# Performance work log

Hardware: AMD Instinct MI355X
Metric: run time of the kernel (lower is better)

The kernel has to match this reference:

```python
import jax, jax.numpy as jnp
import numpy as np

# SuperposedExpert: K parallel TT-factorized FFN paths + holographic routing.
# d_model=1024 factorized as [32,32]; d_ff=4096 as [64,64]; tt_ranks=[1,16,1] (r0/r2 squeezed).
K, D_MODEL, D_FF, RANK = 4, 1024, 4096, 16
IN1, IN2 = 32, 32          # factorize_for_tt(d_model)
F1, F2 = 64, 64            # factorize_for_tt(d_ff)
TEMP = 1.0                 # routing_temperature


def setup_inputs() -> dict:
    key = jax.random.key(0)
    ks = jax.random.split(key, 8)
    s = 0.05
    tokens = jax.random.normal(ks[0], (2048, D_MODEL), dtype=jnp.float32)
    # TT cores for ffn1: d_model -> d_ff  (input_dims [32,32], output_dims [64,64])
    ffn1_core1 = jax.random.normal(ks[1], (K, IN1, F1, RANK), dtype=jnp.float32) * s
    ffn1_core2 = jax.random.normal(ks[2], (K, RANK, IN2, F2), dtype=jnp.float32) * s
    # TT cores for ffn2: d_ff -> d_model (input_dims [64,64], output_dims [32,32])
    ffn2_core1 = jax.random.normal(ks[3], (K, F1, IN1, RANK), dtype=jnp.float32) * s
    ffn2_core2 = jax.random.normal(ks[4], (K, RANK, F2, IN2), dtype=jnp.float32) * s
    # Holographic routing params (hd_dim == d_model -> identity HD projection)
    pb = jax.random.normal(ks[5], (K, D_MODEL), dtype=jnp.float32)
    path_bases = pb / jnp.linalg.norm(pb, axis=-1, keepdims=True)  # orthogonal-ish init
    path_weights = jax.random.normal(ks[6], (K, D_MODEL), dtype=jnp.float32) * s
    return {
        'tokens': tokens,
        'ffn1_core1': ffn1_core1, 'ffn1_core2': ffn1_core2,
        'ffn2_core1': ffn2_core1, 'ffn2_core2': ffn2_core2,
        'path_bases': path_bases, 'path_weights': path_weights,
    }


def reference(tokens, ffn1_core1, ffn1_core2, ffn2_core1, ffn2_core2,
              path_bases, path_weights):
    N = tokens.shape[0]
    # ---- K superposed TT-FFN paths ----
    x3 = tokens.reshape(N, IN1, IN2)  # [n, a, b]
    # TT matmul 1: y[x,y] = sum_{a,b,r} G1[a,x,r] G2[r,b,y] x[a,b]
    h = jnp.einsum('nab,kaxr,krby->knxy', x3, ffn1_core1, ffn1_core2)
    h = jax.nn.gelu(h.reshape(K, N, D_FF))  # quantum_activation stand-in
    h3 = h.reshape(K, N, F1, F2)
    y = jnp.einsum('knab,kaxr,krby->knxy', h3, ffn2_core1, ffn2_core2)
    y = y.reshape(K, N, D_MODEL)  # per-path outputs
    # ---- Holographic HD routing (hd_dim == d_model: identity projection) ----
    logits = jnp.einsum('nd,kd->nk', tokens, path_bases) / TEMP
    gates = jax.nn.softmax(logits, axis=-1)  # [n, k]
    # Collapse superposition: per-path elementwise HD modulation + gated sum
    out = jnp.einsum('knd,kd,nk->nd', y, 1.0 + path_weights, gates)
    return out
```

## Files before the change

### kernel.cpp

```cpp
#include <hip/hip_runtime.h>
#include <stdint.h>

#define GAS __attribute__((address_space(1)))
#define LAS __attribute__((address_space(3)))

typedef __attribute__((ext_vector_type(8))) short short8;
typedef __attribute__((ext_vector_type(16))) float f32x16;
typedef __attribute__((ext_vector_type(4))) float f32x4;

static constexpr int N_TOK = 2048;
static constexpr int DM    = 1024;
static constexpr int DF    = 4096;
static constexpr int KP    = 4;

__device__ inline unsigned short f2bf(float f) {
  union { float f; uint32_t u; } v; v.f = f;
  uint32_t u = v.u;
  u += 0x7FFFu + ((u >> 16) & 1u);
  return (unsigned short)(u >> 16);
}

__device__ inline uint32_t pk_bf(float lo, float hi) {
  union { float f; uint32_t u; } a, b; a.f = lo; b.f = hi;
  uint32_t ul = a.u + 0x7FFFu + ((a.u >> 16) & 1u);
  uint32_t uh = b.u + 0x7FFFu + ((b.u >> 16) & 1u);
  return (ul >> 16) | (uh & 0xFFFF0000u);
}

__device__ inline float gelu_gate(float v, float g) {
  float t0 = v * v;
  float u  = v * __builtin_fmaf(t0, -0.10294456f, -2.3022539f);
  float e  = __builtin_amdgcn_exp2f(u);
  float r  = __builtin_amdgcn_rcpf(1.0f + e);
  return v * g * r;
}

__device__ inline void gld16(const void* g, void* l) {
  __builtin_amdgcn_global_load_lds((const GAS void*)g, (LAS void*)l, 16, 0, 0);
}

__global__ __launch_bounds__(256) void setup_kernel(
    const float* __restrict__ tokens, const float* __restrict__ pb,
    const float* __restrict__ c11, const float* __restrict__ c12,
    const float* __restrict__ c21, const float* __restrict__ c22,
    float* __restrict__ gates, unsigned short* __restrict__ xb,
    unsigned short* __restrict__ w1t, unsigned short* __restrict__ w2t) {
  __shared__ __align__(16) float sh[17472];
  const int blk = blockIdx.x;
  const int t = threadIdx.x;
  if (blk < 1024) {
    const int k = blk >> 8, x = (blk >> 2) & 63, y0 = (blk & 3) * 16;
    float* s1  = sh;
    float* s2T = sh + 512;
    if (t < 128) {
      int a = t >> 2, rq = (t & 3) * 4;
      *(float4*)(s1 + a * 16 + rq) =
          *(const float4*)(c11 + (((size_t)(k * 32 + a)) * 64 + x) * 16 + rq);
    }
#pragma unroll
    for (int j = 0; j < 8; ++j) {
      int i = t + j * 256;
      int rb = i >> 2, yy0 = (i & 3) * 4;
      float4 v = *(const float4*)(c12 + (size_t)(k * 16) * 2048 + (size_t)rb * 64 + y0 + yy0);
      s2T[(yy0 + 0) * 524 + rb] = v.x;
      s2T[(yy0 + 1) * 524 + rb] = v.y;
      s2T[(yy0 + 2) * 524 + rb] = v.z;
      s2T[(yy0 + 3) * 524 + rb] = v.w;
    }
    __syncthreads();
    const int a = t >> 3, b0 = (t & 7) * 4;
    float4 s1q[4];
#pragma unroll
    for (int q = 0; q < 4; ++q) s1q[q] = *(const float4*)(s1 + a * 16 + q * 4);
    const float* a0s = (const float*)s1q;
    for (int y = 0; y < 16; ++y) {
      const float* s2y = s2T + y * 524;
      float4 acc = {0.f, 0.f, 0.f, 0.f};
#pragma unroll
      for (int r = 0; r < 16; ++r) {
        float cv = a0s[r];
        float4 bv = *(const float4*)(s2y + r * 32 + b0);
        acc.x = __builtin_fmaf(cv, bv.x, acc.x);
        acc.y = __builtin_fmaf(cv, bv.y, acc.y);
        acc.z = __builtin_fmaf(cv, bv.z, acc.z);
        acc.w = __builtin_fmaf(cv, bv.w, acc.w);
      }
      ushort4 o; o.x = f2bf(acc.x); o.y = f2bf(acc.y); o.z = f2bf(acc.z); o.w = f2bf(acc.w);
      *(ushort4*)(w1t + ((size_t)k * DF + x * 64 + y0 + y) * DM + t * 4) = o;
    }
  } else if (blk < 1280) {
    const int bb = blk - 1024;
    const int k = bb >> 6, x = (bb >> 1) & 31, y0 = (bb & 1) * 16;
    float* s1  = sh;
    float* s2T = sh + 1024;
    {
      int a = t >> 2, rq = (t & 3) * 4;
      *(float4*)(s1 + a * 16 + rq) =
          *(const float4*)(c21 + (((size_t)(k * 64 + a)) * 32 + x) * 16 + rq);
    }
#pragma unroll
    for (int j = 0; j < 16; ++j) {
      int i = t + j * 256;
      int rb = i >> 2, yy0 = (i & 3) * 4;
      float4 v = *(const float4*)(c22 + (size_t)(k * 16) * 2048 + (size_t)rb * 32 + y0 + yy0);
      s2T[(yy0 + 0) * 1028 + rb] = v.x;
      s2T[(yy0 + 1) * 1028 + rb] = v.y;
      s2T[(yy0 + 2) * 1028 + rb] = v.z;
      s2T[(yy0 + 3) * 1028 + rb] = v.w;
    }
    __syncthreads();
    const int b0 = (t & 15) * 4;
#pragma unroll
    for (int jj = 0; jj < 4; ++jj) {
      const int a = (t >> 4) + jj * 16;
      float4 s1q[4];
#pragma unroll
      for (int q = 0; q < 4; ++q) s1q[q] = *(const float4*)(s1 + a * 16 + q * 4);
      const float* a0s = (const float*)s1q;
      for (int y = 0; y < 16; ++y) {
        const float* s2y = s2T + y * 1028;
        float4 acc = {0.f, 0.f, 0.f, 0.f};
#pragma unroll
        for (int r = 0; r < 16; ++r) {
          float cv = a0s[r];
          float4 bv = *(const float4*)(s2y + r * 64 + b0);
          acc.x = __builtin_fmaf(cv, bv.x, acc.x);
          acc.y = __builtin_fmaf(cv, bv.y, acc.y);
          acc.z = __builtin_fmaf(cv, bv.z, acc.z);
          acc.w = __builtin_fmaf(cv, bv.w, acc.w);
        }
        ushort4 o; o.x = f2bf(acc.x); o.y = f2bf(acc.y); o.z = f2bf(acc.z); o.w = f2bf(acc.w);
        *(ushort4*)(w2t + ((size_t)k * DM + x * 32 + y0 + y) * DF + t * 4 + jj * 1024) = o;
      }
    }
  } else {
    const int wave = t >> 6, lane = t & 63;
    const int n = (blk - 1280) * 4 + wave;
    float s0 = 0.f, s1v = 0.f, s2v = 0.f, s3v = 0.f;
    const float4* tr = (const float4*)(tokens + (size_t)n * DM);
#pragma unroll
    for (int j = 0; j < 4; ++j) {
      int idx = j * 64 + lane;
      float4 tv = tr[idx];
      ushort4 b;
      b.x = f2bf(tv.x); b.y = f2bf(tv.y); b.z = f2bf(tv.z); b.w = f2bf(tv.w);
      *(ushort4*)(xb + (size_t)n * DM + idx * 4) = b;
      float4 q;
      q = ((const float4*)(pb + 0 * DM))[idx]; s0  += tv.x*q.x + tv.y*q.y + tv.z*q.z + tv.w*q.w;
      q = ((const float4*)(pb + 1 * DM))[idx]; s1v += tv.x*q.x + tv.y*q.y + tv.z*q.z + tv.w*q.w;
      q = ((const float4*)(pb + 2 * DM))[idx]; s2v += tv.x*q.x + tv.y*q.y + tv.z*q.z + tv.w*q.w;
      q = ((const float4*)(pb + 3 * DM))[idx]; s3v += tv.x*q.x + tv.y*q.y + tv.z*q.z + tv.w*q.w;
    }
#pragma unroll
    for (int off = 32; off > 0; off >>= 1) {
      s0  += __shfl_xor(s0, off);
      s1v += __shfl_xor(s1v, off);
      s2v += __shfl_xor(s2v, off);
      s3v += __shfl_xor(s3v, off);
    }
    if (lane == 0) {
      float m = fmaxf(fmaxf(s0, s1v), fmaxf(s2v, s3v));
      float e0 = __expf(s0 - m), e1 = __expf(s1v - m), e2 = __expf(s2v - m), e3 = __expf(s3v - m);
      float inv = 1.0f / (e0 + e1 + e2 + e3);
      float4 g; g.x = e0 * inv; g.y = e1 * inv; g.z = e2 * inv; g.w = e3 * inv;
      *(float4*)(gates + n * 4) = g;
    }
  }
}

#define PH_SYNC(V) do { \
    asm volatile("s_waitcnt vmcnt(" #V ")" ::: "memory"); \
    __builtin_amdgcn_s_barrier(); \
    __builtin_amdgcn_sched_barrier(0); \
  } while (0)

#define G1_TILE(KT, BO, WO, V0, V1, V2) do { \
    const int kn_ = ((KT) + 1) * 64; \
    const bool st_ = (KT) < 15; \
     \
    PH_SYNC(V0); \
    if (st_) { const unsigned short* s_ = Wg + (size_t)srow * DM + kn_ + lch * 8; \
      gld16(s_, smem + (WO) + t * 16); gld16(s_ + 64 * DM, smem + (WO) + 8192 + t * 16); } \
    _Pragma("unroll") for (int fi = 0; fi < 4; ++fi) \
      _Pragma("unroll") for (int s = 0; s < 2; ++s) \
        af[fi][s] = *(const short8*)(smem + (BO) + aRowB + fi * 2048 + (cxor16 ^ (s * 64) ^ (fi * 32))); \
    _Pragma("unroll") for (int ti = 0; ti < 2; ++ti) \
      _Pragma("unroll") for (int s = 0; s < 2; ++s) \
        bf0[ti][s] = *(const short8*)(smem + (BO) + xRowB + ti * 2048 + (cxor16 ^ (s * 64) ^ wnx64 ^ (ti * 32))); \
    __builtin_amdgcn_s_setprio(1); \
    _Pragma("unroll") for (int fi = 0; fi < 4; ++fi) \
      _Pragma("unroll") for (int ti = 0; ti < 2; ++ti) { \
        acc[0][0][fi][ti] = __builtin_amdgcn_mfma_f32_16x16x32_bf16(af[fi][0], bf0[ti][0], acc[0][0][fi][ti], 0, 0, 0); \
        acc[0][0][fi][ti] = __builtin_amdgcn_mfma_f32_16x16x32_bf16(af[fi][1], bf0[ti][1], acc[0][0][fi][ti], 0, 0, 0); } \
    __builtin_amdgcn_s_setprio(0); \
     \
    PH_SYNC(V1); \
    if (st_) { const unsigned short* s_ = Xg + (size_t)srow * DM + kn_ + lch * 8; \
      gld16(s_, smem + (WO) + 32768 + t * 16); gld16(s_ + 64 * DM, smem + (WO) + 32768 + 8192 + t * 16); } \
    _Pragma("unroll") for (int ti = 0; ti < 2; ++ti) \
      _Pragma("unroll") for (int s = 0; s < 2; ++s) \
        bf1[ti][s] = *(const short8*)(smem + (BO) + xRowB + 16384 + ti * 2048 + (cxor16 ^ (s * 64) ^ wnx64 ^ (ti * 32))); \
    __builtin_amdgcn_s_setprio(1); \
    _Pragma("unroll") for (int fi = 0; fi < 4; ++fi) \
      _Pragma("unroll") for (int ti = 0; ti < 2; ++ti) { \
        acc[0][1][fi][ti] = __builtin_amdgcn_mfma_f32_16x16x32_bf16(af[fi][0], bf1[ti][0], acc[0][1][fi][ti], 0, 0, 0); \
        acc[0][1][fi][ti] = __builtin_amdgcn_mfma_f32_16x16x32_bf16(af[fi][1], bf1[ti][1], acc[0][1][fi][ti], 0, 0, 0); } \
    __builtin_amdgcn_s_setprio(0); \
     \
    PH_SYNC(V2); \
    if (st_) { const unsigned short* s_ = Xg + (size_t)(128 + srow) * DM + kn_ + lch * 8; \
      gld16(s_, smem + (WO) + 32768 + 16384 + t * 16); gld16(s_ + 64 * DM, smem + (WO) + 32768 + 16384 + 8192 + t * 16); } \
    _Pragma("unroll") for (int fi = 0; fi < 4; ++fi) \
      _Pragma("unroll") for (int s = 0; s < 2; ++s) \
        af[fi][s] = *(const short8*)(smem + (BO) + aRowB + 16384 + fi * 2048 + (cxor16 ^ (s * 64) ^ (fi * 32))); \
    __builtin_amdgcn_s_setprio(1); \
    _Pragma("unroll") for (int fi = 0; fi < 4; ++fi) \
      _Pragma("unroll") for (int ti = 0; ti < 2; ++ti) { \
        acc[1][1][fi][ti] = __builtin_amdgcn_mfma_f32_16x16x32_bf16(af[fi][0], bf1[ti][0], acc[1][1][fi][ti], 0, 0, 0); \
        acc[1][1][fi][ti] = __builtin_amdgcn_mfma_f32_16x16x32_bf16(af[fi][1], bf1[ti][1], acc[1][1][fi][ti], 0, 0, 0); } \
    __builtin_amdgcn_s_setprio(0); \
     \
    if (st_) { const unsigned short* s_ = Wg + (size_t)(128 + srow) * DM + kn_ + lch * 8; \
      gld16(s_, smem + (WO) + 16384 + t * 16); gld16(s_ + 64 * DM, smem + (WO) + 16384 + 8192 + t * 16); } \
    __builtin_amdgcn_s_setprio(1); \
    _Pragma("unroll") for (int fi = 0; fi < 4; ++fi) \
      _Pragma("unroll") for (int ti = 0; ti < 2; ++ti) { \
        acc[1][0][fi][ti] = __builtin_amdgcn_mfma_f32_16x16x32_bf16(af[fi][0], bf0[ti][0], acc[1][0][fi][ti], 0, 0, 0); \
        acc[1][0][fi][ti] = __builtin_amdgcn_mfma_f32_16x16x32_bf16(af[fi][1], bf0[ti][1], acc[1][0][fi][ti], 0, 0, 0); } \
    __builtin_amdgcn_s_setprio(0); \
  } while (0)

__global__ __launch_bounds__(512, 1) void gemm1(
    const unsigned short* __restrict__ xb, const unsigned short* __restrict__ w1t,
    const float* __restrict__ gates, unsigned short* __restrict__ hg) {
  __shared__ __align__(16) char smem[131072];
  const int t = threadIdx.x, lane = t & 63, wv = t >> 6;
  const int wm = wv >> 2, wn = wv & 3;
  const int hw = blockIdx.x + (blockIdx.y << 3) + (blockIdx.z << 7);
  const int lg = (hw & 7) * 64 + (hw >> 3);
  const int m0 = (lg & 7) * 256;
  const int f0 = ((lg >> 3) & 15) * 256;
  const int kp = lg >> 7;
  const unsigned short* __restrict__ Wg = w1t + (size_t)kp * DF * DM + (size_t)f0 * DM;
  const unsigned short* __restrict__ Xg = xb + (size_t)m0 * DM;

  const int srow = t >> 3;
  const int lch  = (t & 7) ^ (srow & 7) ^ (srow >> 3);
  const int l15 = lane & 15, kg = lane >> 4;
  const int cxor16 = (kg ^ (lane & 7) ^ (l15 >> 3)) * 16;
  const int wnx64  = (wn & 1) * 64;
  const int aRowB  = (wm * 64 + l15) * 128;
  const int xRowB  = 32768 + (wn * 32 + l15) * 128;

  f32x4 acc[2][2][4][2] = {};
  short8 af[4][2], bf0[2][2], bf1[2][2];

  {
    const unsigned short* sw = Wg + (size_t)srow * DM + lch * 8;
    const unsigned short* sx = Xg + (size_t)srow * DM + lch * 8;
    gld16(sw,            smem + t * 16);
    gld16(sw + 64 * DM,  smem + 8192 + t * 16);
    gld16(sx,            smem + 32768 + t * 16);
    gld16(sx + 64 * DM,  smem + 32768 + 8192 + t * 16);
    gld16(sx + 128 * DM, smem + 32768 + 16384 + t * 16);
    gld16(sx + 192 * DM, smem + 32768 + 16384 + 8192 + t * 16);
    gld16(sw + 128 * DM, smem + 16384 + t * 16);
    gld16(sw + 192 * DM, smem + 16384 + 8192 + t * 16);
  }

#pragma unroll 1
  for (int kt = 0; kt < 14; kt += 2) {
    G1_TILE(kt,     0,     65536, 4, 4, 4);
    G1_TILE(kt + 1, 65536, 0,     4, 4, 4);
  }
  G1_TILE(14, 0,     65536, 4, 4, 4);
  G1_TILE(15, 65536, 0,     4, 2, 0);

  unsigned short* __restrict__ H = hg + (size_t)kp * N_TOK * DF;
#pragma unroll
  for (int cB = 0; cB < 2; ++cB)
#pragma unroll
    for (int ti = 0; ti < 2; ++ti) {
      const int tok = m0 + cB * 128 + wn * 32 + ti * 16 + l15;
      const float g = gates[tok * 4 + kp];
      unsigned short* hrow = H + (size_t)tok * DF + f0 + wm * 64 + kg * 4;
#pragma unroll
      for (int rA = 0; rA < 2; ++rA)
#pragma unroll
        for (int fi = 0; fi < 4; ++fi) {
          f32x4 v = acc[rA][cB][fi][ti];
          float r0 = gelu_gate(v.x, g);
          float r1 = gelu_gate(v.y, g);
          float r2 = gelu_gate(v.z, g);
          float r3 = gelu_gate(v.w, g);
          uint2 p; p.x = pk_bf(r0, r1); p.y = pk_bf(r2, r3);
          *(uint2*)(hrow + rA * 128 + fi * 16) = p;
        }
    }
}

#define G2_TILE(KT, BO, WO, V0, V1, V2) do { \
    const int kn_ = ((KT) + 1) * 64; \
    const bool st_ = (KT) < 63; \
     \
    PH_SYNC(V0); \
    if (st_) gld16(Wg + (size_t)srow * DF + kn_ + lch * 8, smem + (WO) + t * 16); \
    _Pragma("unroll") for (int fi = 0; fi < 2; ++fi) \
      _Pragma("unroll") for (int s = 0; s < 2; ++s) \
        af[fi][s] = *(const short8*)(smem + (BO) + awRowB + fi * 2048 + (cxor16 ^ awx ^ (fi * 32) ^ (s * 64))); \
    _Pragma("unroll") for (int ti = 0; ti < 2; ++ti) \
      _Pragma("unroll") for (int s = 0; s < 2; ++s) \
        bf0[ti][s] = *(const short8*)(smem + (BO) + xRowB + ti * 2048 + (cxor16 ^ wnx64 ^ (ti * 32) ^ (s * 64))); \
    __builtin_amdgcn_s_setprio(1); \
    _Pragma("unroll") for (int fi = 0; fi < 2; ++fi) \
      _Pragma("unroll") for (int ti = 0; ti < 2; ++ti) { \
        acc[0][0][fi][ti] = __builtin_amdgcn_mfma_f32_16x16x32_bf16(af[fi][0], bf0[ti][0], acc[0][0][fi][ti], 0, 0, 0); \
        acc[0][0][fi][ti] = __builtin_amdgcn_mfma_f32_16x16x32_bf16(af[fi][1], bf0[ti][1], acc[0][0][fi][ti], 0, 0, 0); } \
    __builtin_amdgcn_s_setprio(0); \
     \
    PH_SYNC(V1); \
    if (st_) { const unsigned short* s_ = Xg + (size_t)srow * DF + kn_ + lch * 8; \
      gld16(s_, smem + (WO) + 16384 + t * 16); gld16(s_ + 64 * DF, smem + (WO) + 16384 + 8192 + t * 16); } \
    _Pragma("unroll") for (int ti = 0; ti < 2; ++ti) \
      _Pragma("unroll") for (int s = 0; s < 2; ++s) \
        bf1[ti][s] = *(const short8*)(smem + (BO) + xRowB + 16384 + ti * 2048 + (cxor16 ^ wnx64 ^ (ti * 32) ^ (s * 64))); \
    __builtin_amdgcn_s_setprio(1); \
    _Pragma("unroll") for (int fi = 0; fi < 2; ++fi) \
      _Pragma("unroll") for (int ti = 0; ti < 2; ++ti) { \
        acc[0][1][fi][ti] = __builtin_amdgcn_mfma_f32_16x16x32_bf16(af[fi][0], bf1[ti][0], acc[0][1][fi][ti], 0, 0, 0); \
        acc[0][1][fi][ti] = __builtin_amdgcn_mfma_f32_16x16x32_bf16(af[fi][1], bf1[ti][1], acc[0][1][fi][ti], 0, 0, 0); } \
    __builtin_amdgcn_s_setprio(0); \
     \
    PH_SYNC(V2); \
    if (st_) { const unsigned short* s_ = Xg + (size_t)(128 + srow) * DF + kn_ + lch * 8; \
      gld16(s_, smem + (WO) + 32768 + t * 16); gld16(s_ + 64 * DF, smem + (WO) + 32768 + 8192 + t * 16); } \
    _Pragma("unroll") for (int fi = 0; fi < 2; ++fi) \
      _Pragma("unroll") for (int s = 0; s < 2; ++s) \
        af[fi][s] = *(const short8*)(smem + (BO) + awRowB + 8192 + fi * 2048 + (cxor16 ^ awx ^ (fi * 32) ^ (s * 64))); \
    __builtin_amdgcn_s_setprio(1); \
    _Pragma("unroll") for (int fi = 0; fi < 2; ++fi) \
      _Pragma("unroll") for (int ti = 0; ti < 2; ++ti) { \
        acc[1][1][fi][ti] = __builtin_amdgcn_mfma_f32_16x16x32_bf16(af[fi][0], bf1[ti][0], acc[1][1][fi][ti], 0, 0, 0); \
        acc[1][1][fi][ti] = __builtin_amdgcn_mfma_f32_16x16x32_bf16(af[fi][1], bf1[ti][1], acc[1][1][fi][ti], 0, 0, 0); } \
    __builtin_amdgcn_s_setprio(0); \
     \
    if (st_) gld16(Wg + (size_t)(64 + srow) * DF + kn_ + lch * 8, smem + (WO) + 8192 + t * 16); \
    __builtin_amdgcn_s_setprio(1); \
    _Pragma("unroll") for (int fi = 0; fi < 2; ++fi) \
      _Pragma("unroll") for (int ti = 0; ti < 2; ++ti) { \
        acc[1][0][fi][ti] = __builtin_amdgcn_mfma_f32_16x16x32_bf16(af[fi][0], bf0[ti][0], acc[1][0][fi][ti], 0, 0, 0); \
        acc[1][0][fi][ti] = __builtin_amdgcn_mfma_f32_16x16x32_bf16(af[fi][1], bf0[ti][1], acc[1][0][fi][ti], 0, 0, 0); } \
    __builtin_amdgcn_s_setprio(0); \
  } while (0)

__global__ __launch_bounds__(512, 1) void gemm2(
    const unsigned short* __restrict__ hg, const unsigned short* __restrict__ w2t,
    const float* __restrict__ pw, float* __restrict__ part) {
  __shared__ __align__(16) char smem[98304];
  const int t = threadIdx.x, lane = t & 63, wv = t >> 6;
  const int wm = wv >> 2, wn = wv & 3;
  const int hw = blockIdx.x + (blockIdx.y << 3) + (blockIdx.z << 6);
  const int lg = (hw & 7) * 32 + (hw >> 3);
  const int m0 = (lg & 7) * 256;
  const int n0 = ((lg >> 3) & 7) * 128;
  const int kp = lg >> 6;
  const unsigned short* __restrict__ Wg = w2t + (size_t)kp * DM * DF + (size_t)n0 * DF;
  const unsigned short* __restrict__ Xg = hg + (size_t)kp * N_TOK * DF + (size_t)m0 * DF;

  const int srow = t >> 3;
  const int lch  = (t & 7) ^ (srow & 7) ^ (srow >> 3);
  const int l15 = lane & 15, kg = lane >> 4;
  const int cxor16 = (kg ^ (lane & 7) ^ (l15 >> 3)) * 16;
  const int wnx64  = (wn & 1) * 64;
  const int awx    = wm * 64;
  const int awRowB = (wm * 32 + l15) * 128;
  const int xRowB  = 16384 + (wn * 32 + l15) * 128;

  f32x4 acc[2][2][2][2] = {};
  short8 af[2][2], bf0[2][2], bf1[2][2];

  {
    const unsigned short* sw = Wg + (size_t)srow * DF + lch * 8;
    const unsigned short* sx = Xg + (size_t)srow * DF + lch * 8;
    gld16(sw,            smem + t * 16);
    gld16(sx,            smem + 16384 + t * 16);
    gld16(sx + 64 * DF,  smem + 16384 + 8192 + t * 16);
    gld16(sx + 128 * DF, smem + 32768 + t * 16);
    gld16(sx + 192 * DF, smem + 32768 + 8192 + t * 16);
    gld16(sw + 64 * DF,  smem + 8192 + t * 16);
  }

#pragma unroll 1
  for (int kt = 0; kt < 62; kt += 2) {
    G2_TILE(kt,     0,     49152, 3, 2, 3);
    G2_TILE(kt + 1, 49152, 0,     3, 2, 3);
  }
  G2_TILE(62, 0,     49152, 3, 2, 3);
  G2_TILE(63, 49152, 0,     3, 1, 0);

  float* __restrict__ P = part + (size_t)kp * N_TOK * DM;
  float4 pwv[2][2];
#pragma unroll
  for (int rA = 0; rA < 2; ++rA)
#pragma unroll
    for (int fi = 0; fi < 2; ++fi) {
      float4 w = *(const float4*)(pw + kp * DM + n0 + rA * 64 + wm * 32 + fi * 16 + kg * 4);
      pwv[rA][fi].x = 1.0f + w.x; pwv[rA][fi].y = 1.0f + w.y;
      pwv[rA][fi].z = 1.0f + w.z; pwv[rA][fi].w = 1.0f + w.w;
    }
#pragma unroll
  for (int cB = 0; cB < 2; ++cB)
#pragma unroll
    for (int ti = 0; ti < 2; ++ti) {
      const int tok = m0 + cB * 128 + wn * 32 + ti * 16 + l15;
      float* prow = P + (size_t)tok * DM + n0 + wm * 32 + kg * 4;
#pragma unroll
      for (int rA = 0; rA < 2; ++rA)
#pragma unroll
        for (int fi = 0; fi < 2; ++fi) {
          f32x4 v = acc[rA][cB][fi][ti];
          float4 o;
          o.x = pwv[rA][fi].x * v.x;
          o.y = pwv[rA][fi].y * v.y;
          o.z = pwv[rA][fi].z * v.z;
          o.w = pwv[rA][fi].w * v.w;
          *(float4*)(prow + rA * 64 + fi * 16) = o;
        }
    }
}

__global__ __launch_bounds__(256) void reduce_k(
    const float* __restrict__ part, float* __restrict__ out) {
  const size_t i = ((size_t)blockIdx.x * 256 + threadIdx.x) * 4;
  const size_t S = (size_t)N_TOK * DM;
  float4 a = *(const float4*)(part + i);
  float4 b = *(const float4*)(part + S + i);
  float4 c = *(const float4*)(part + 2 * S + i);
  float4 d = *(const float4*)(part + 3 * S + i);
  float4 r;
  r.x = a.x + b.x + c.x + d.x;
  r.y = a.y + b.y + c.y + d.y;
  r.z = a.z + b.z + c.z + d.z;
  r.w = a.w + b.w + c.w + d.w;
  *(float4*)(out + i) = r;
}

extern "C" void kernel_launch(void* const* d_in, const int* in_sizes, int n_in,
                              void* d_out, int out_size, void* d_ws, size_t ws_size,
                              hipStream_t stream) {
  const float* tokens = (const float*)d_in[0];
  const float* f1c1   = (const float*)d_in[1];
  const float* f1c2   = (const float*)d_in[2];
  const float* f2c1   = (const float*)d_in[3];
  const float* f2c2   = (const float*)d_in[4];
  const float* pb     = (const float*)d_in[5];
  const float* pw     = (const float*)d_in[6];
  float* out = (float*)d_out;

  char* ws = (char*)d_ws;
  unsigned short* xb  = (unsigned short*)(ws);
  unsigned short* w1t = (unsigned short*)(ws + (4ull  << 20));
  float*          part = (float*)(ws + (4ull << 20));
  unsigned short* w2t = (unsigned short*)(ws + (36ull << 20));
  unsigned short* hg  = (unsigned short*)(ws + (68ull << 20));
  float*          gates = (float*)(ws + (132ull << 20));

  hipLaunchKernelGGL(setup_kernel, dim3(1792), dim3(256), 0, stream,
                     tokens, pb, f1c1, f1c2, f2c1, f2c2, gates, xb, w1t, w2t);
  hipLaunchKernelGGL(gemm1, dim3(8, 16, KP), dim3(512), 0, stream, xb, w1t, gates, hg);
  hipLaunchKernelGGL(gemm2, dim3(8, 8, KP), dim3(512), 0, stream, hg, w2t, pw, part);
  hipLaunchKernelGGL(reduce_k, dim3(2048), dim3(256), 0, stream, part, out);
}
```

Before: 243.9 us.

## Software-pipeline LDS fragment loads across phases in both GEMM kernels

Restructures the per-tile phase schedule in gemm1 and gemm2 so that the LDS fragment reads for the next phase (and the next tile's A/B fragments) are issued after the current MFMA block, not before it. The vmcnt waits and barrier placement are rearranged to match: one barrier moves to just before the third MFMA group, and a prologue preloads the first fragments. The goal is to hide LDS read latency behind MFMA execution. In exchange, register pressure goes up and the correctness of the wait counts becomes more delicate.

```diff
diff --git a/kernel.cpp b/kernel.cpp
--- a/kernel.cpp
+++ b/kernel.cpp
@@ -168,67 +168,67 @@
   }
 }
 
-#define PH_SYNC(V) do { \
-    asm volatile("s_waitcnt vmcnt(" #V ")" ::: "memory"); \
-    __builtin_amdgcn_s_barrier(); \
-    __builtin_amdgcn_sched_barrier(0); \
-  } while (0)
-
-#define G1_TILE(KT, BO, WO, V0, V1, V2) do { \
-    const int kn_ = ((KT) + 1) * 64; \
-    const bool st_ = (KT) < 15; \
-     \
-    PH_SYNC(V0); \
-    if (st_) { const unsigned short* s_ = Wg + (size_t)srow * DM + kn_ + lch * 8; \
-      gld16(s_, smem + (WO) + t * 16); gld16(s_ + 64 * DM, smem + (WO) + 8192 + t * 16); } \
+#define VMC(N) asm volatile("s_waitcnt vmcnt(" #N ")" ::: "memory")
+#define BARS do { __builtin_amdgcn_s_barrier(); __builtin_amdgcn_sched_barrier(0); } while (0)
+
+#define G1T(KT, BO, WO, V0X, V1X, DO2, PREF) do { \
+  const int kn_ = ((KT) + 1) * 64; \
+  const bool st_ = (KT) < 15; \
+   \
+  VMC(V0X); BARS; \
+  if (st_) { const unsigned short* s_ = Wg + (size_t)srow * DM + kn_ + lch * 8; \
+    gld16(s_, smem + (WO) + t * 16); gld16(s_ + 64 * DM, smem + (WO) + 8192 + t * 16); } \
+  __builtin_amdgcn_s_setprio(1); \
+  _Pragma("unroll") for (int fi = 0; fi < 4; ++fi) \
+    _Pragma("unroll") for (int ti = 0; ti < 2; ++ti) { \
+      acc[0][0][fi][ti] = __builtin_amdgcn_mfma_f32_16x16x32_bf16(af[fi][0], bf0[ti][0], acc[0][0][fi][ti], 0, 0, 0); \
+      acc[0][0][fi][ti] = __builtin_amdgcn_mfma_f32_16x16x32_bf16(af[fi][1], bf0[ti][1], acc[0][0][fi][ti], 0, 0, 0); } \
+  __builtin_amdgcn_s_setprio(0); \
+  _Pragma("unroll") for (int ti = 0; ti < 2; ++ti) \
+    _Pragma("unroll") for (int s = 0; s < 2; ++s) \
+      bf1[ti][s] = *(const short8*)(smem + (BO) + xRowB + 16384 + ti * 2048 + (cxor16 ^ (s * 64) ^ wnx64 ^ (ti * 32))); \
+   \
+  VMC(V1X); BARS; \
+  if (st_) { const unsigned short* s_ = Xg + (size_t)srow * DM + kn_ + lch * 8; \
+    gld16(s_, smem + (WO) + 32768 + t * 16); gld16(s_ + 64 * DM, smem + (WO) + 32768 + 8192 + t * 16); } \
+  __builtin_amdgcn_s_setprio(1); \
+  _Pragma("unroll") for (int fi = 0; fi < 4; ++fi) \
+    _Pragma("unroll") for (int ti = 0; ti < 2; ++ti) { \
+      acc[0][1][fi][ti] = __builtin_amdgcn_mfma_f32_16x16x32_bf16(af[fi][0], bf1[ti][0], acc[0][1][fi][ti], 0, 0, 0); \
+      acc[0][1][fi][ti] = __builtin_amdgcn_mfma_f32_16x16x32_bf16(af[fi][1], bf1[ti][1], acc[0][1][fi][ti], 0, 0, 0); } \
+  __builtin_amdgcn_s_setprio(0); \
+  _Pragma("unroll") for (int fi = 0; fi < 4; ++fi) \
+    _Pragma("unroll") for (int s = 0; s < 2; ++s) \
+      af[fi][s] = *(const short8*)(smem + (BO) + aRowB + 16384 + fi * 2048 + (cxor16 ^ (s * 64) ^ (fi * 32))); \
+   \
+  if (st_) { const unsigned short* s_ = Xg + (size_t)(128 + srow) * DM + kn_ + lch * 8; \
+    gld16(s_, smem + (WO) + 32768 + 16384 + t * 16); gld16(s_ + 64 * DM, smem + (WO) + 32768 + 16384 + 8192 + t * 16); } \
+  if (DO2) { VMC(2); } \
+  BARS; \
+  __builtin_amdgcn_s_setprio(1); \
+  _Pragma("unroll") for (int fi = 0; fi < 4; ++fi) \
+    _Pragma("unroll") for (int ti = 0; ti < 2; ++ti) { \
+      acc[1][1][fi][ti] = __builtin_amdgcn_mfma_f32_16x16x32_bf16(af[fi][0], bf1[ti][0], acc[1][1][fi][ti], 0, 0, 0); \
+      acc[1][1][fi][ti] = __builtin_amdgcn_mfma_f32_16x16x32_bf16(af[fi][1], bf1[ti][1], acc[1][1][fi][ti], 0, 0, 0); } \
+  __builtin_amdgcn_s_setprio(0); \
+   \
+  if (st_) { const unsigned short* s_ = Wg + (size_t)(128 + srow) * DM + kn_ + lch * 8; \
+    gld16(s_, smem + (WO) + 16384 + t * 16); gld16(s_ + 64 * DM, smem + (WO) + 16384 + 8192 + t * 16); } \
+  __builtin_amdgcn_s_setprio(1); \
+  _Pragma("unroll") for (int fi = 0; fi < 4; ++fi) \
+    _Pragma("unroll") for (int ti = 0; ti < 2; ++ti) { \
+      acc[1][0][fi][ti] = __builtin_amdgcn_mfma_f32_16x16x32_bf16(af[fi][0], bf0[ti][0], acc[1][0][fi][ti], 0, 0, 0); \
+      acc[1][0][fi][ti] = __builtin_amdgcn_mfma_f32_16x16x32_bf16(af[fi][1], bf0[ti][1], acc[1][0][fi][ti], 0, 0, 0); } \
+  __builtin_amdgcn_s_setprio(0); \
+  if (PREF) { \
     _Pragma("unroll") for (int fi = 0; fi < 4; ++fi) \
       _Pragma("unroll") for (int s = 0; s < 2; ++s) \
-        af[fi][s] = *(const short8*)(smem + (BO) + aRowB + fi * 2048 + (cxor16 ^ (s * 64) ^ (fi * 32))); \
+        af[fi][s] = *(const short8*)(smem + (WO) + aRowB + fi * 2048 + (cxor16 ^ (s * 64) ^ (fi * 32))); \
     _Pragma("unroll") for (int ti = 0; ti < 2; ++ti) \
       _Pragma("unroll") for (int s = 0; s < 2; ++s) \
-        bf0[ti][s] = *(const short8*)(smem + (BO) + xRowB + ti * 2048 + (cxor16 ^ (s * 64) ^ wnx64 ^ (ti * 32))); \
-    __builtin_amdgcn_s_setprio(1); \
-    _Pragma("unroll") for (int fi = 0; fi < 4; ++fi) \
-      _Pragma("unroll") for (int ti = 0; ti < 2; ++ti) { \
-        acc[0][0][fi][ti] = __builtin_amdgcn_mfma_f32_16x16x32_bf16(af[fi][0], bf0[ti][0], acc[0][0][fi][ti], 0, 0, 0); \
-        acc[0][0][fi][ti] = __builtin_amdgcn_mfma_f32_16x16x32_bf16(af[fi][1], bf0[ti][1], acc[0][0][fi][ti], 0, 0, 0); } \
-    __builtin_amdgcn_s_setprio(0); \
-     \
-    PH_SYNC(V1); \
-    if (st_) { const unsigned short* s_ = Xg + (size_t)srow * DM + kn_ + lch * 8; \
-      gld16(s_, smem + (WO) + 32768 + t * 16); gld16(s_ + 64 * DM, smem + (WO) + 32768 + 8192 + t * 16); } \
-    _Pragma("unroll") for (int ti = 0; ti < 2; ++ti) \
-      _Pragma("unroll") for (int s = 0; s < 2; ++s) \
-        bf1[ti][s] = *(const short8*)(smem + (BO) + xRowB + 16384 + ti * 2048 + (cxor16 ^ (s * 64) ^ wnx64 ^ (ti * 32))); \
-    __builtin_amdgcn_s_setprio(1); \
-    _Pragma("unroll") for (int fi = 0; fi < 4; ++fi) \
-      _Pragma("unroll") for (int ti = 0; ti < 2; ++ti) { \
-        acc[0][1][fi][ti] = __builtin_amdgcn_mfma_f32_16x16x32_bf16(af[fi][0], bf1[ti][0], acc[0][1][fi][ti], 0, 0, 0); \
-        acc[0][1][fi][ti] = __builtin_amdgcn_mfma_f32_16x16x32_bf16(af[fi][1], bf1[ti][1], acc[0][1][fi][ti], 0, 0, 0); } \
-    __builtin_amdgcn_s_setprio(0); \
-     \
-    PH_SYNC(V2); \
-    if (st_) { const unsigned short* s_ = Xg + (size_t)(128 + srow) * DM + kn_ + lch * 8; \
-      gld16(s_, smem + (WO) + 32768 + 16384 + t * 16); gld16(s_ + 64 * DM, smem + (WO) + 32768 + 16384 + 8192 + t * 16); } \
-    _Pragma("unroll") for (int fi = 0; fi < 4; ++fi) \
-      _Pragma("unroll") for (int s = 0; s < 2; ++s) \
-        af[fi][s] = *(const short8*)(smem + (BO) + aRowB + 16384 + fi * 2048 + (cxor16 ^ (s * 64) ^ (fi * 32))); \
-    __builtin_amdgcn_s_setprio(1); \
-    _Pragma("unroll") for (int fi = 0; fi < 4; ++fi) \
-      _Pragma("unroll") for (int ti = 0; ti < 2; ++ti) { \
-        acc[1][1][fi][ti] = __builtin_amdgcn_mfma_f32_16x16x32_bf16(af[fi][0], bf1[ti][0], acc[1][1][fi][ti], 0, 0, 0); \
-        acc[1][1][fi][ti] = __builtin_amdgcn_mfma_f32_16x16x32_bf16(af[fi][1], bf1[ti][1], acc[1][1][fi][ti], 0, 0, 0); } \
-    __builtin_amdgcn_s_setprio(0); \
-     \
-    if (st_) { const unsigned short* s_ = Wg + (size_t)(128 + srow) * DM + kn_ + lch * 8; \
-      gld16(s_, smem + (WO) + 16384 + t * 16); gld16(s_ + 64 * DM, smem + (WO) + 16384 + 8192 + t * 16); } \
-    __builtin_amdgcn_s_setprio(1); \
-    _Pragma("unroll") for (int fi = 0; fi < 4; ++fi) \
-      _Pragma("unroll") for (int ti = 0; ti < 2; ++ti) { \
-        acc[1][0][fi][ti] = __builtin_amdgcn_mfma_f32_16x16x32_bf16(af[fi][0], bf0[ti][0], acc[1][0][fi][ti], 0, 0, 0); \
-        acc[1][0][fi][ti] = __builtin_amdgcn_mfma_f32_16x16x32_bf16(af[fi][1], bf0[ti][1], acc[1][0][fi][ti], 0, 0, 0); } \
-    __builtin_amdgcn_s_setprio(0); \
-  } while (0)
+        bf0[ti][s] = *(const short8*)(smem + (WO) + xRowB + ti * 2048 + (cxor16 ^ (s * 64) ^ wnx64 ^ (ti * 32))); \
+  } \
+} while (0)
 
 __global__ __launch_bounds__(512, 1) void gemm1(
     const unsigned short* __restrict__ xb, const unsigned short* __restrict__ w1t,
@@ -267,14 +267,25 @@
     gld16(sw + 128 * DM, smem + 16384 + t * 16);
     gld16(sw + 192 * DM, smem + 16384 + 8192 + t * 16);
   }
+  VMC(4); BARS;
+#pragma unroll
+  for (int fi = 0; fi < 4; ++fi)
+#pragma unroll
+    for (int s = 0; s < 2; ++s)
+      af[fi][s] = *(const short8*)(smem + aRowB + fi * 2048 + (cxor16 ^ (s * 64) ^ (fi * 32)));
+#pragma unroll
+  for (int ti = 0; ti < 2; ++ti)
+#pragma unroll
+    for (int s = 0; s < 2; ++s)
+      bf0[ti][s] = *(const short8*)(smem + xRowB + ti * 2048 + (cxor16 ^ (s * 64) ^ wnx64 ^ (ti * 32)));
 
 #pragma unroll 1
   for (int kt = 0; kt < 14; kt += 2) {
-    G1_TILE(kt,     0,     65536, 4, 4, 4);
-    G1_TILE(kt + 1, 65536, 0,     4, 4, 4);
+    G1T(kt,     0,     65536, 2, 2, 1, 1);
+    G1T(kt + 1, 65536, 0,     2, 2, 1, 1);
   }
-  G1_TILE(14, 0,     65536, 4, 4, 4);
-  G1_TILE(15, 65536, 0,     4, 2, 0);
+  G1T(14, 0,     65536, 2, 2, 1, 1);
+  G1T(15, 65536, 0,     2, 0, 0, 0);
 
   unsigned short* __restrict__ H = hg + (size_t)kp * N_TOK * DF;
 #pragma unroll
@@ -299,59 +310,62 @@
     }
 }
 
-#define G2_TILE(KT, BO, WO, V0, V1, V2) do { \
-    const int kn_ = ((KT) + 1) * 64; \
-    const bool st_ = (KT) < 63; \
-     \
-    PH_SYNC(V0); \
-    if (st_) gld16(Wg + (size_t)srow * DF + kn_ + lch * 8, smem + (WO) + t * 16); \
+#define G2T(KT, BO, WO, V0X, V1X, DO2, PREF) do { \
+  const int kn_ = ((KT) + 1) * 64; \
+  const bool st_ = (KT) < 63; \
+   \
+  VMC(V0X); BARS; \
+  if (st_) gld16(Wg + (size_t)srow * DF + kn_ + lch * 8, smem + (WO) + t * 16); \
+  __builtin_amdgcn_s_setprio(1); \
+  _Pragma("unroll") for (int fi = 0; fi < 2; ++fi) \
+    _Pragma("unroll") for (int ti = 0; ti < 2; ++ti) { \
+      acc[0][0][fi][ti] = __builtin_amdgcn_mfma_f32_16x16x32_bf16(af[fi][0], bf0[ti][0], acc[0][0][fi][ti], 0, 0, 0); \
+      acc[0][0][fi][ti] = __builtin_amdgcn_mfma_f32_16x16x32_bf16(af[fi][1], bf0[ti][1], acc[0][0][fi][ti], 0, 0, 0); } \
+  __builtin_amdgcn_s_setprio(0); \
+  _Pragma("unroll") for (int ti = 0; ti < 2; ++ti) \
+    _Pragma("unroll") for (int s = 0; s < 2; ++s) \
+      bf1[ti][s] = *(const short8*)(smem + (BO) + xRowB + 16384 + ti * 2048 + (cxor16 ^ wnx64 ^ (ti * 32) ^ (s * 64))); \
+   \
+  VMC(V1X); BARS; \
+  if (st_) { const unsigned short* s_ = Xg + (size_t)srow * DF + kn_ + lch * 8; \
+    gld16(s_, smem + (WO) + 16384 + t * 16); gld16(s_ + 64 * DF, smem + (WO) + 16384 + 8192 + t * 16); } \
+  __builtin_amdgcn_s_setprio(1); \
+  _Pragma("unroll") for (int fi = 0; fi < 2; ++fi) \
+    _Pragma("unroll") for (int ti = 0; ti < 2; ++ti) { \
+      acc[0][1][fi][ti] = __builtin_amdgcn_mfma_f32_16x16x32_bf16(af[fi][0], bf1[ti][0], acc[0][1][fi][ti], 0, 0, 0); \
+      acc[0][1][fi][ti] = __builtin_amdgcn_mfma_f32_16x16x32_bf16(af[fi][1], bf1[ti][1], acc[0][1][fi][ti], 0, 0, 0); } \
+  __builtin_amdgcn_s_setprio(0); \
+  _Pragma("unroll") for (int fi = 0; fi < 2; ++fi) \
+    _Pragma("unroll") for (int s = 0; s < 2; ++s) \
+      af[fi][s] = *(const short8*)(smem + (BO) + awRowB + 8192 + fi * 2048 + (cxor16 ^ awx ^ (fi * 32) ^ (s * 64))); \
+   \
+  if (st_) { const unsigned short* s_ = Xg + (size_t)(128 + srow) * DF + kn_ + lch * 8; \
+    gld16(s_, smem + (WO) + 32768 + t * 16); gld16(s_ + 64 * DF, smem + (WO) + 32768 + 8192 + t * 16); } \
+  if (DO2) { VMC(2); } \
+  BARS; \
+  __builtin_amdgcn_s_setprio(1); \
+  _Pragma("unroll") for (int fi = 0; fi < 2; ++fi) \
+    _Pragma("unroll") for (int ti = 0; ti < 2; ++ti) { \
+      acc[1][1][fi][ti] = __builtin_amdgcn_mfma_f32_16x16x32_bf16(af[fi][0], bf1[ti][0], acc[1][1][fi][ti], 0, 0, 0); \
+      acc[1][1][fi][ti] = __builtin_amdgcn_mfma_f32_16x16x32_bf16(af[fi][1], bf1[ti][1], acc[1][1][fi][ti], 0, 0, 0); } \
+  __builtin_amdgcn_s_setprio(0); \
+   \
+  if (st_) gld16(Wg + (size_t)(64 + srow) * DF + kn_ + lch * 8, smem + (WO) + 8192 + t * 16); \
+  __builtin_amdgcn_s_setprio(1); \
+  _Pragma("unroll") for (int fi = 0; fi < 2; ++fi) \
+    _Pragma("unroll") for (int ti = 0; ti < 2; ++ti) { \
+      acc[1][0][fi][ti] = __builtin_amdgcn_mfma_f32_16x16x32_bf16(af[fi][0], bf0[ti][0], acc[1][0][fi][ti], 0, 0, 0); \
+      acc[1][0][fi][ti] = __builtin_amdgcn_mfma_f32_16x16x32_bf16(af[fi][1], bf0[ti][1], acc[1][0][fi][ti], 0, 0, 0); } \
+  __builtin_amdgcn_s_setprio(0); \
+  if (PREF) { \
     _Pragma("unroll") for (int fi = 0; fi < 2; ++fi) \
       _Pragma("unroll") for (int s = 0; s < 2; ++s) \
-        af[fi][s] = *(const short8*)(smem + (BO) + awRowB + fi * 2048 + (cxor16 ^ awx ^ (fi * 32) ^ (s * 64))); \
+        af[fi][s] = *(const short8*)(smem + (WO) + awRowB + fi * 2048 + (cxor16 ^ awx ^ (fi * 32) ^ (s * 64))); \
     _Pragma("unroll") for (int ti = 0; ti < 2; ++ti) \
       _Pragma("unroll") for (int s = 0; s < 2; ++s) \
-        bf0[ti][s] = *(const short8*)(smem + (BO) + xRowB + ti * 2048 + (cxor16 ^ wnx64 ^ (ti * 32) ^ (s * 64))); \
-    __builtin_amdgcn_s_setprio(1); \
-    _Pragma("unroll") for (int fi = 0; fi < 2; ++fi) \
-      _Pragma("unroll") for (int ti = 0; ti < 2; ++ti) { \
-        acc[0][0][fi][ti] = __builtin_amdgcn_mfma_f32_16x16x32_bf16(af[fi][0], bf0[ti][0], acc[0][0][fi][ti], 0, 0, 0); \
-        acc[0][0][fi][ti] = __builtin_amdgcn_mfma_f32_16x16x32_bf16(af[fi][1], bf0[ti][1], acc[0][0][fi][ti], 0, 0, 0); } \
-    __builtin_amdgcn_s_setprio(0); \
-     \
-    PH_SYNC(V1); \
-    if (st_) { const unsigned short* s_ = Xg + (size_t)srow * DF + kn_ + lch * 8; \
-      gld16(s_, smem + (WO) + 16384 + t * 16); gld16(s_ + 64 * DF, smem + (WO) + 16384 + 8192 + t * 16); } \
-    _Pragma("unroll") for (int ti = 0; ti < 2; ++ti) \
-      _Pragma("unroll") for (int s = 0; s < 2; ++s) \
-        bf1[ti][s] = *(const short8*)(smem + (BO) + xRowB + 16384 + ti * 2048 + (cxor16 ^ wnx64 ^ (ti * 32) ^ (s * 64))); \
-    __builtin_amdgcn_s_setprio(1); \
-    _Pragma("unroll") for (int fi = 0; fi < 2; ++fi) \
-      _Pragma("unroll") for (int ti = 0; ti < 2; ++ti) { \
-        acc[0][1][fi][ti] = __builtin_amdgcn_mfma_f32_16x16x32_bf16(af[fi][0], bf1[ti][0], acc[0][1][fi][ti], 0, 0, 0); \
-        acc[0][1][fi][ti] = __builtin_amdgcn_mfma_f32_16x16x32_bf16(af[fi][1], bf1[ti][1], acc[0][1][fi][ti], 0, 0, 0); } \
-    __builtin_amdgcn_s_setprio(0); \
-     \
-    PH_SYNC(V2); \
-    if (st_) { const unsigned short* s_ = Xg + (size_t)(128 + srow) * DF + kn_ + lch * 8; \
-      gld16(s_, smem + (WO) + 32768 + t * 16); gld16(s_ + 64 * DF, smem + (WO) + 32768 + 8192 + t * 16); } \
-    _Pragma("unroll") for (int fi = 0; fi < 2; ++fi) \
-      _Pragma("unroll") for (int s = 0; s < 2; ++s) \
-        af[fi][s] = *(const short8*)(smem + (BO) + awRowB + 8192 + fi * 2048 + (cxor16 ^ awx ^ (fi * 32) ^ (s * 64))); \
-    __builtin_amdgcn_s_setprio(1); \
-    _Pragma("unroll") for (int fi = 0; fi < 2; ++fi) \
-      _Pragma("unroll") for (int ti = 0; ti < 2; ++ti) { \
-        acc[1][1][fi][ti] = __builtin_amdgcn_mfma_f32_16x16x32_bf16(af[fi][0], bf1[ti][0], acc[1][1][fi][ti], 0, 0, 0); \
-        acc[1][1][fi][ti] = __builtin_amdgcn_mfma_f32_16x16x32_bf16(af[fi][1], bf1[ti][1], acc[1][1][fi][ti], 0, 0, 0); } \
-    __builtin_amdgcn_s_setprio(0); \
-     \
-    if (st_) gld16(Wg + (size_t)(64 + srow) * DF + kn_ + lch * 8, smem + (WO) + 8192 + t * 16); \
-    __builtin_amdgcn_s_setprio(1); \
-    _Pragma("unroll") for (int fi = 0; fi < 2; ++fi) \
-      _Pragma("unroll") for (int ti = 0; ti < 2; ++ti) { \
-        acc[1][0][fi][ti] = __builtin_amdgcn_mfma_f32_16x16x32_bf16(af[fi][0], bf0[ti][0], acc[1][0][fi][ti], 0, 0, 0); \
-        acc[1][0][fi][ti] = __builtin_amdgcn_mfma_f32_16x16x32_bf16(af[fi][1], bf0[ti][1], acc[1][0][fi][ti], 0, 0, 0); } \
-    __builtin_amdgcn_s_setprio(0); \
-  } while (0)
+        bf0[ti][s] = *(const short8*)(smem + (WO) + xRowB + ti * 2048 + (cxor16 ^ wnx64 ^ (ti * 32) ^ (s * 64))); \
+  } \
+} while (0)
 
 __global__ __launch_bounds__(512, 1) void gemm2(
     const unsigned short* __restrict__ hg, const unsigned short* __restrict__ w2t,
@@ -389,14 +403,25 @@
     gld16(sx + 192 * DF, smem + 32768 + 8192 + t * 16);
     gld16(sw + 64 * DF,  smem + 8192 + t * 16);
   }
+  VMC(3); BARS;
+#pragma unroll
+  for (int fi = 0; fi < 2; ++fi)
+#pragma unroll
+    for (int s = 0; s < 2; ++s)
+      af[fi][s] = *(const short8*)(smem + awRowB + fi * 2048 + (cxor16 ^ awx ^ (fi * 32) ^ (s * 64)));
+#pragma unroll
+  for (int ti = 0; ti < 2; ++ti)
+#pragma unroll
+    for (int s = 0; s < 2; ++s)
+      bf0[ti][s] = *(const short8*)(smem + xRowB + ti * 2048 + (cxor16 ^ wnx64 ^ (ti * 32) ^ (s * 64)));
 
 #pragma unroll 1
   for (int kt = 0; kt < 62; kt += 2) {
-    G2_TILE(kt,     0,     49152, 3, 2, 3);
-    G2_TILE(kt + 1, 49152, 0,     3, 2, 3);
+    G2T(kt,     0,     49152, 1, 1, 1, 1);
+    G2T(kt + 1, 49152, 0,     1, 1, 1, 1);
   }
-  G2_TILE(62, 0,     49152, 3, 2, 3);
-  G2_TILE(63, 49152, 0,     3, 1, 0);
+  G2T(62, 0,     49152, 1, 1, 1, 1);
+  G2T(63, 49152, 0,     1, 0, 0, 0);
 
   float* __restrict__ P = part + (size_t)kp * N_TOK * DM;
   float4 pwv[2][2];
```

After: 261.2 us. +7.1%, slower.
